# Kernel optimization log

Hardware: AMD Instinct MI355X
Metric: run time of the kernel (lower is better)

The kernel has to match this reference:

```python
import jax, jax.numpy as jnp
import numpy as np

MARGIN = 0.5
EPS = 1e-8  # torch F.cosine_similarity eps


def setup_inputs() -> dict:
    key = jax.random.key(0)
    k1, k2 = jax.random.split(key)
    N, D = 4096, 1024
    img_emb = jax.random.normal(k1, (N, D), dtype=jnp.float32)
    txt_emb = jax.random.normal(k2, (N, D), dtype=jnp.float32)
    return {"img_emb": img_emb, "txt_emb": txt_emb}


def reference(img_emb, txt_emb):
    N = img_emb.shape[0]
    # norms, clamped at eps exactly like torch cosine_similarity
    img_norm = jnp.maximum(jnp.linalg.norm(img_emb, axis=-1), EPS)  # [N]
    txt_norm = jnp.maximum(jnp.linalg.norm(txt_emb, axis=-1), EPS)  # [N]

    # positive: rowwise cosine similarity
    pos_sim = jnp.sum(img_emb * txt_emb, axis=-1) / (img_norm * txt_norm)  # [N]

    # negative: full pairwise cosine sim as normalized GEMM (avoids N,N,D tensor)
    sim = (img_emb @ txt_emb.T) / (img_norm[:, None] * txt_norm[None, :])  # [N, N]
    sim = sim * (1.0 - jnp.eye(N, dtype=sim.dtype))  # fill_diagonal_(0.0)

    loss_positive = jnp.mean((1.0 - pos_sim) ** 2)
    loss_negative = jnp.mean(jnp.maximum(sim - MARGIN, 0.0) ** 2)
    return loss_positive + loss_negative
```

## Files before the change

kernel.cpp:

```cpp
#include <hip/hip_runtime.h>
#include <hip/hip_bf16.h>

typedef unsigned char  u8;
typedef unsigned int   u32;
typedef __attribute__((ext_vector_type(4))) int   int4v;
typedef __attribute__((ext_vector_type(8))) int   int8v;
typedef __attribute__((ext_vector_type(4))) float float4v;

#define N_ROWS 4096
#define DIM    1024
#define MARGIN 0.5f
#define FP4_SCALE 32.0f
#define INV_SCALE2 (1.0f / (FP4_SCALE * FP4_SCALE))
#define ROWB 512

#define BM 128
#define BN 128
#define NBLK ((N_ROWS / BM) * (N_ROWS / BN))


__device__ __forceinline__ float wave_reduce(float v) {
    #pragma unroll
    for (int off = 32; off > 0; off >>= 1) v += __shfl_xor(v, off, 64);
    return v;
}

__device__ __forceinline__ void gl_lds16(const void* g, void* l) {
    __builtin_amdgcn_global_load_lds(
        (const __attribute__((address_space(1))) void*)g,
        (__attribute__((address_space(3))) void*)l,
        16, 0, 0);
}

__device__ __forceinline__ u32 q4(float v) {
    float a = fabsf(v);
    u32 c = (a >= 0.25f) + (a >= 0.75f) + (a >= 1.25f) + (a >= 1.75f)
          + (a >= 2.5f)  + (a >= 3.5f)  + (a >= 5.0f);
    return c | (v < 0.0f ? 8u : 0u);
}


__global__ __launch_bounds__(256) void rowprep(
        const float* __restrict__ img, const float* __restrict__ txt,
        u8* __restrict__ imgn, u8* __restrict__ txtn,
        float* __restrict__ pospart, u32* __restrict__ ticket) {
    const int t = threadIdx.x;
    const int wave = t >> 6, lane = t & 63;
    const int row  = blockIdx.x * 2 + (wave >> 1);
    const int half = wave & 1;

    if (blockIdx.x == 0 && t == 0) *ticket = 0u;

    const float4* ip = (const float4*)img + (size_t)row * 256 + half * 128;
    const float4* tp = (const float4*)txt + (size_t)row * 256 + half * 128;

    float4 iv[2], tv[2];
    #pragma unroll
    for (int k = 0; k < 2; ++k) {
        iv[k] = ip[k * 64 + lane];
        tv[k] = tp[k * 64 + lane];
    }

    float sii = 0.f, si2 = 0.f, st2 = 0.f;
    #pragma unroll
    for (int k = 0; k < 2; ++k) {
        sii += iv[k].x*tv[k].x + iv[k].y*tv[k].y + iv[k].z*tv[k].z + iv[k].w*tv[k].w;
        si2 += iv[k].x*iv[k].x + iv[k].y*iv[k].y + iv[k].z*iv[k].z + iv[k].w*iv[k].w;
        st2 += tv[k].x*tv[k].x + tv[k].y*tv[k].y + tv[k].z*tv[k].z + tv[k].w*tv[k].w;
    }

    sii = wave_reduce(sii);
    si2 = wave_reduce(si2);
    st2 = wave_reduce(st2);

    __shared__ float red[4][3];
    if (lane == 0) { red[wave][0] = sii; red[wave][1] = si2; red[wave][2] = st2; }
    __syncthreads();
    const int pw = wave ^ 1;
    sii += red[pw][0];
    si2 += red[pw][1];
    st2 += red[pw][2];

    float ni = fmaxf(sqrtf(si2), 1e-8f);
    float nt = fmaxf(sqrtf(st2), 1e-8f);
    float ii = 1.0f / ni, it = 1.0f / nt;
    float si = FP4_SCALE * ii, st = FP4_SCALE * it;

    u32 pa = 0, pb = 0;
    #pragma unroll
    for (int k = 0; k < 2; ++k) {
        pa |= q4(iv[k].x * si) << (k*16 + 0);  pa |= q4(iv[k].y * si) << (k*16 + 4);
        pa |= q4(iv[k].z * si) << (k*16 + 8);  pa |= q4(iv[k].w * si) << (k*16 + 12);
        pb |= q4(tv[k].x * st) << (k*16 + 0);  pb |= q4(tv[k].y * st) << (k*16 + 4);
        pb |= q4(tv[k].z * st) << (k*16 + 8);  pb |= q4(tv[k].w * st) << (k*16 + 12);
    }
    ((u32*)imgn)[(size_t)row * 128 + half * 64 + lane] = pa;
    ((u32*)txtn)[(size_t)row * 128 + half * 64 + lane] = pb;

    if (half == 0 && lane == 0) {
        float d = 1.0f - sii * ii * it;
        pospart[row] = d * d;
    }
}


__global__ __launch_bounds__(256) void negloss(
        const u8* __restrict__ A, const u8* __restrict__ B,
        const float* __restrict__ pospart,
        float* __restrict__ negpart, u32* __restrict__ ticket,
        float* __restrict__ out) {
    __shared__ __align__(16) u8 sA[2][BM * 64];
    __shared__ __align__(16) u8 sB[2][BN * 64];

    const int tid = threadIdx.x;
    const int wave = tid >> 6, lane = tid & 63;
    const int wr = wave >> 1, wc = wave & 1;
    const int rA0 = blockIdx.y * BM;
    const int rB0 = blockIdx.x * BN;

    const int lr = lane >> 2;
    const int lc = (lane & 3) ^ (lr & 3);
    const u8* gA = A + (size_t)(rA0 + wave * 32 + lr) * ROWB + lc * 16;
    const u8* gB = B + (size_t)(rB0 + wave * 32 + lr) * ROWB + lc * 16;
    const int ub = wave * 2048;

    const int mrow = lane & 15;
    const int rsw  = ((lane >> 4) ^ (lane & 3)) * 16;

    float4v acc[4][4] = {};

    {
        gl_lds16(gA,            (char*)sA[0] + ub);
        gl_lds16(gA + 16*ROWB,  (char*)sA[0] + ub + 1024);
        gl_lds16(gB,            (char*)sB[0] + ub);
        gl_lds16(gB + 16*ROWB,  (char*)sB[0] + ub + 1024);
    }
    __syncthreads();

    int cur = 0;
    #pragma unroll
    for (int it = 0; it < 8; ++it) {
        if (it < 7) {
            const int nb = cur ^ 1;
            gl_lds16(gA + (it+1)*64,            (char*)sA[nb] + ub);
            gl_lds16(gA + 16*ROWB + (it+1)*64,  (char*)sA[nb] + ub + 1024);
            gl_lds16(gB + (it+1)*64,            (char*)sB[nb] + ub);
            gl_lds16(gB + 16*ROWB + (it+1)*64,  (char*)sB[nb] + ub + 1024);
        }

        int8v af[4], bf[4];
        #pragma unroll
        for (int i = 0; i < 4; ++i) {
            int ra = wr * 64 + i * 16 + mrow;
            int rb = wc * 64 + i * 16 + mrow;
            int4v a = *(const int4v*)(sA[cur] + ra * 64 + rsw);
            int4v b = *(const int4v*)(sB[cur] + rb * 64 + rsw);
            af[i] = int8v{a[0], a[1], a[2], a[3], 0, 0, 0, 0};
            bf[i] = int8v{b[0], b[1], b[2], b[3], 0, 0, 0, 0};
        }
        #pragma unroll
        for (int i = 0; i < 4; ++i)
            #pragma unroll
            for (int j = 0; j < 4; ++j)
                acc[i][j] = __builtin_amdgcn_mfma_scale_f32_16x16x128_f8f6f4(
                    af[i], bf[j], acc[i][j],
                    4 , 4 ,
                    0, 0x7F7F7F7F ,
                    0, 0x7F7F7F7F );

        __syncthreads();
        cur ^= 1;
    }

    float local = 0.0f;
    const int crow = (lane >> 4) * 4;
    const int ccol = lane & 15;
    #pragma unroll
    for (int i = 0; i < 4; ++i) {
        int gi_base = rA0 + wr * 64 + i * 16 + crow;
        #pragma unroll
        for (int j = 0; j < 4; ++j) {
            int gj = rB0 + wc * 64 + j * 16 + ccol;
            #pragma unroll
            for (int r = 0; r < 4; ++r) {
                float sim = acc[i][j][r] * INV_SCALE2;
                float h = fmaxf(sim - MARGIN, 0.0f);
                if (gi_base + r == gj) h = 0.0f;
                local += h * h;
            }
        }
    }

    local = wave_reduce(local);
    __shared__ float part[4];
    __shared__ int lastflag;
    if (lane == 0) part[wave] = local;
    __syncthreads();
    if (tid == 0) {
        float bsum = part[0] + part[1] + part[2] + part[3];
        int bid = blockIdx.y * gridDim.x + blockIdx.x;
        negpart[bid] = bsum;
        __threadfence();
        u32 prev = atomicAdd(ticket, 1u);
        lastflag = (prev == NBLK - 1);
    }
    __syncthreads();
    if (!lastflag) return;

    __threadfence();
    float sp = 0.f, sn = 0.f;
    #pragma unroll
    for (int i = 0; i < 16; ++i) sp += pospart[i * 256 + tid];
    #pragma unroll
    for (int i = 0; i < 4;  ++i) sn += negpart[i * 256 + tid];
    sp = wave_reduce(sp);
    sn = wave_reduce(sn);
    __shared__ float rp[4], rn[4];
    if (lane == 0) { rp[wave] = sp; rn[wave] = sn; }
    __syncthreads();
    if (tid == 0) {
        float pos = rp[0] + rp[1] + rp[2] + rp[3];
        float neg = rn[0] + rn[1] + rn[2] + rn[3];
        out[0] = pos * (1.0f / (float)N_ROWS)
               + neg * (1.0f / ((float)N_ROWS * (float)N_ROWS));
    }
}


extern "C" void kernel_launch(void* const* d_in, const int* in_sizes, int n_in,
                              void* d_out, int out_size, void* d_ws, size_t ws_size,
                              hipStream_t stream) {
    const float* img = (const float*)d_in[0];
    const float* txt = (const float*)d_in[1];
    float* out = (float*)d_out;

    u8* imgn = (u8*)d_ws;
    u8* txtn = imgn + (size_t)N_ROWS * ROWB;
    float* pospart = (float*)(txtn + (size_t)N_ROWS * ROWB);
    float* negpart = pospart + 4096;
    u32* ticket = (u32*)(negpart + 1024);

    rowprep<<<N_ROWS / 2, 256, 0, stream>>>(img, txt, imgn, txtn, pospart, ticket);
    negloss<<<dim3(N_ROWS / BN, N_ROWS / BM), 256, 0, stream>>>(
        imgn, txtn, pospart, negpart, ticket, out);
}
```

Before: 108.4 us.

## Load FP4 MFMA operands directly from global memory, dropping LDS staging

Removes the double-buffered LDS staging (global_load_lds plus barriers) in the negative-loss GEMM kernel. Each wave now reads its MFMA A/B fragments straight from global memory, relying on L2/L1 since the quantized operands are small (4 MB total). This drops the LDS traffic and per-iteration __syncthreads. In exchange, operand reuse across waves in a block goes through cache instead of shared memory, and there is no explicit prefetch overlap.

After: 130.9 us. +20.8%, slower.

```diff
diff --git a/kernel.cpp b/kernel.cpp
--- a/kernel.cpp
+++ b/kernel.cpp
@@ -23,13 +23,6 @@
     #pragma unroll
     for (int off = 32; off > 0; off >>= 1) v += __shfl_xor(v, off, 64);
     return v;
-}
-
-__device__ __forceinline__ void gl_lds16(const void* g, void* l) {
-    __builtin_amdgcn_global_load_lds(
-        (const __attribute__((address_space(1))) void*)g,
-        (__attribute__((address_space(3))) void*)l,
-        16, 0, 0);
 }
 
 __device__ __forceinline__ u32 q4(float v) {
@@ -109,52 +102,33 @@
         const float* __restrict__ pospart,
         float* __restrict__ negpart, u32* __restrict__ ticket,
         float* __restrict__ out) {
-    __shared__ __align__(16) u8 sA[2][BM * 64];
-    __shared__ __align__(16) u8 sB[2][BN * 64];
-
     const int tid = threadIdx.x;
     const int wave = tid >> 6, lane = tid & 63;
     const int wr = wave >> 1, wc = wave & 1;
     const int rA0 = blockIdx.y * BM;
     const int rB0 = blockIdx.x * BN;
 
-    const int lr = lane >> 2;
-    const int lc = (lane & 3) ^ (lr & 3);
-    const u8* gA = A + (size_t)(rA0 + wave * 32 + lr) * ROWB + lc * 16;
-    const u8* gB = B + (size_t)(rB0 + wave * 32 + lr) * ROWB + lc * 16;
-    const int ub = wave * 2048;
-
     const int mrow = lane & 15;
-    const int rsw  = ((lane >> 4) ^ (lane & 3)) * 16;
+    const int kg   = lane >> 4;
+
+    const u8* pA[4];
+    const u8* pB[4];
+    #pragma unroll
+    for (int i = 0; i < 4; ++i) {
+        pA[i] = A + (size_t)(rA0 + wr * 64 + i * 16 + mrow) * ROWB + kg * 16;
+        pB[i] = B + (size_t)(rB0 + wc * 64 + i * 16 + mrow) * ROWB + kg * 16;
+    }
 
     float4v acc[4][4] = {};
 
-    {
-        gl_lds16(gA,            (char*)sA[0] + ub);
-        gl_lds16(gA + 16*ROWB,  (char*)sA[0] + ub + 1024);
-        gl_lds16(gB,            (char*)sB[0] + ub);
-        gl_lds16(gB + 16*ROWB,  (char*)sB[0] + ub + 1024);
-    }
-    __syncthreads();
-
-    int cur = 0;
-    #pragma unroll
-    for (int it = 0; it < 8; ++it) {
-        if (it < 7) {
-            const int nb = cur ^ 1;
-            gl_lds16(gA + (it+1)*64,            (char*)sA[nb] + ub);
-            gl_lds16(gA + 16*ROWB + (it+1)*64,  (char*)sA[nb] + ub + 1024);
-            gl_lds16(gB + (it+1)*64,            (char*)sB[nb] + ub);
-            gl_lds16(gB + 16*ROWB + (it+1)*64,  (char*)sB[nb] + ub + 1024);
-        }
-
+    #pragma unroll
+    for (int ks = 0; ks < 8; ++ks) {
+        const int off = ks * 64;
         int8v af[4], bf[4];
         #pragma unroll
         for (int i = 0; i < 4; ++i) {
-            int ra = wr * 64 + i * 16 + mrow;
-            int rb = wc * 64 + i * 16 + mrow;
-            int4v a = *(const int4v*)(sA[cur] + ra * 64 + rsw);
-            int4v b = *(const int4v*)(sB[cur] + rb * 64 + rsw);
+            int4v a = *(const int4v*)(pA[i] + off);
+            int4v b = *(const int4v*)(pB[i] + off);
             af[i] = int8v{a[0], a[1], a[2], a[3], 0, 0, 0, 0};
             bf[i] = int8v{b[0], b[1], b[2], b[3], 0, 0, 0, 0};
         }
@@ -167,9 +141,6 @@
                     4 , 4 ,
                     0, 0x7F7F7F7F ,
                     0, 0x7F7F7F7F );
-
-        __syncthreads();
-        cur ^= 1;
     }
 
     float local = 0.0f;
```
